# Optimization experiments

Hardware: AMD Instinct MI355X
Metric: run time of the kernel (lower is better)

Reference implementation:

```python
import jax, jax.numpy as jnp
import numpy as np

I, H, B, T, C = 256, 1024, 64, 256, 60


def setup_inputs() -> dict:
    key = jax.random.key(0)
    ks = jax.random.split(key, 7)
    s_ih = 1.0 / np.sqrt(H)
    return {
        "inputs": jax.random.normal(ks[0], (B, T, I), dtype=jnp.float32),
        "W_ih": jax.random.uniform(ks[1], (4 * H, I), jnp.float32, -s_ih, s_ih),
        "W_hh": jax.random.uniform(ks[2], (4 * H, H), jnp.float32, -s_ih, s_ih),
        "b_ih": jax.random.uniform(ks[3], (4 * H,), jnp.float32, -s_ih, s_ih),
        "b_hh": jax.random.uniform(ks[4], (4 * H,), jnp.float32, -s_ih, s_ih),
        "fc_w": jax.random.uniform(ks[5], (C, H), jnp.float32, -s_ih, s_ih),
        "fc_b": jax.random.uniform(ks[6], (C,), jnp.float32, -s_ih, s_ih),
    }


def reference(inputs, W_ih, W_hh, b_ih, b_hh, fc_w, fc_b):
    # Precompute input projections for all timesteps: [T, B, 4H]
    x_proj = jnp.einsum('bti,gi->tbg', inputs, W_ih) + b_ih + b_hh

    def step(carry, xg):
        h, c = carry
        gates = xg + h @ W_hh.T  # [B, 4H]
        i, f, g, o = jnp.split(gates, 4, axis=-1)  # PyTorch gate order i,f,g,o
        i = jax.nn.sigmoid(i)
        f = jax.nn.sigmoid(f)
        g = jnp.tanh(g)
        o = jax.nn.sigmoid(o)
        c_new = f * c + i * g
        h_new = o * jnp.tanh(c_new)
        return (h_new, c_new), None

    h0 = jnp.zeros((B, H), inputs.dtype)
    c0 = jnp.zeros((B, H), inputs.dtype)
    (h_last, _), _ = jax.lax.scan(step, (h0, c0), x_proj)

    logits = h_last @ fc_w.T + fc_b  # [B, C]
    return jax.nn.log_softmax(logits, axis=-1)
```

## Files before the change

### kernel.cpp

```cpp
#include <hip/hip_runtime.h>
#include <hip/hip_bf16.h>

typedef unsigned short u16;
typedef unsigned int u32;
typedef unsigned long long u64;
typedef __attribute__((ext_vector_type(8))) short short8;
typedef __attribute__((ext_vector_type(4))) float floatx4;

#define I_DIM 256
#define H_DIM 1024
#define B_DIM 64
#define T_DIM 256
#define C_DIM 60
#define NWG   128
#define UPW   8
#define BSTR  20
#define PACE  5

#define LDS_W_OFF    0
#define LDS_BIAS_OFF 81920
#define LDS_PACC_OFF 82048
#define LDS_FLAG_OFF 123008
#define LDS_TOTAL    123040

#define WS_XSWZ   0u
#define WS_HSWZ   8388608u
#define WS_HLAST  41943040u

#define LSBM 0x0001000100010001ull

__device__ __forceinline__ u16 f2bf(float f) {
    u32 u = __float_as_uint(f);
    u32 r = (u + 0x7fffu + ((u >> 16) & 1u)) >> 16;
    return (u16)r;
}
__device__ __forceinline__ float fsig(float x) { return 1.0f / (1.0f + __expf(-x)); }
__device__ __forceinline__ float ftanh(float x) { return 2.0f * fsig(2.0f * x) - 1.0f; }

union hfrag { short8 s; u64 q[2]; };

extern "C" __global__ void prep_x(const float* __restrict__ in, u16* __restrict__ xswz) {
    int o = blockIdx.x * 256 + threadIdx.x;
    int m = o & 15, q = (o >> 4) & 3, s = (o >> 6) & 7, mt = (o >> 9) & 3, t = o >> 11;
    int b = mt * 16 + m, k = s * 32 + q * 8;
    const float* src = in + ((size_t)(b * T_DIM + t)) * I_DIM + k;
    float4 v0 = *(const float4*)src;
    float4 v1 = *(const float4*)(src + 4);
    short8 val;
    val[0] = (short)f2bf(v0.x); val[1] = (short)f2bf(v0.y);
    val[2] = (short)f2bf(v0.z); val[3] = (short)f2bf(v0.w);
    val[4] = (short)f2bf(v1.x); val[5] = (short)f2bf(v1.y);
    val[6] = (short)f2bf(v1.z); val[7] = (short)f2bf(v1.w);
    *(short8*)(xswz + (size_t)o * 8) = val;
}

extern "C" __global__ void __launch_bounds__(512, 2) lstm_scan(
    const u16* __restrict__ xswz, u16* hswz,
    const float* __restrict__ Wih, const float* __restrict__ Whh,
    const float* __restrict__ bih, const float* __restrict__ bhh,
    float* hlast)
{
    extern __shared__ char lds[];
    u16*   Wlds = (u16*)(lds + LDS_W_OFF);
    float* bias = (float*)(lds + LDS_BIAS_OFF);
    float* pacc = (float*)(lds + LDS_PACC_OFF);
    int*   sbf  = (int*)(lds + LDS_FLAG_OFF);

    const int j    = blockIdx.x;
    const int tid  = threadIdx.x;
    const int lane = tid & 63;
    const int w    = tid >> 6;
    const int s    = w >> 1;
    const int ws   = w & 1;

    for (int i = 0; i < 10; ++i) {
        int wu = tid + i * 512;
        int nn = wu & 15, q = (wu >> 4) & 3, rest = wu >> 6;
        int sg = rest % 40, nt = rest / 40;
        int n = nt * 16 + nn;
        int g = n >> 3, uu = n & 7;
        int r = g * H_DIM + j * UPW + uu;
        int kb = sg * 32 + q * 8;
        const float* src = (kb < I_DIM) ? (Wih + (size_t)r * I_DIM + kb)
                                        : (Whh + (size_t)r * H_DIM + (kb - I_DIM));
        short8 val;
        #pragma unroll
        for (int e = 0; e < 8; ++e) val[e] = (short)f2bf(src[e]);
        *(short8*)(Wlds + (size_t)wu * 8) = val;
    }
    if (tid < 32) {
        int n = tid, g = n >> 3, uu = n & 7;
        int r = g * H_DIM + j * UPW + uu;
        bias[n] = bih[r] + bhh[r];
    }
    if (tid < 4) sbf[tid] = 0;
    __syncthreads();

    const int m16 = lane & 15, q4 = lane >> 4;
    const int sl    = ws * 64 + lane;
    const int pw_pm = sl >> 3;
    const int pw_uu = sl & 7;
    float creg = 0.0f;
    float* pacc_s = pacc + s * (2 * 64 * BSTR);
    int*   flag   = sbf + s;

    hfrag a[20];

    #pragma unroll
    for (int ss = 0; ss < 4; ++ss) {
        int sg = ws * 4 + ss;
        a[ss].s = *(const short8*)(xswz
            + (size_t)(((s * 8 + sg) * 4 + q4) * 16 + m16) * 8);
    }
    #pragma unroll
    for (int ss = 4; ss < 20; ++ss) {
        int sgh = ws * 16 + (ss - 4);
        a[ss].s = *(const short8*)(hswz
            + (size_t)(((s * 32 + sgh) * 4 + q4) * 16 + m16) * 8);
    }

    for (int t = 0; t < T_DIM; ++t) {
        const u16* hbase = hswz + (size_t)t * (B_DIM * H_DIM);
        u16*       hnext = hswz + (size_t)(t + 1) * (B_DIM * H_DIM);
        const u16* xnext = xswz + (size_t)(t + 1) * (B_DIM * I_DIM);
        const int  En    = (t % 13) + 1;
        const u64  Eq    = (u64)(En & 1) | ((u64)((En >> 1) & 1) << 16)
                         | ((u64)((En >> 2) & 1) << 32) | ((u64)((En >> 3) & 1) << 48);
        const int  Ep    = ((t + 1) % 13) + 1;

        floatx4 acc[2];
        acc[0] = (floatx4){0.f, 0.f, 0.f, 0.f};
        acc[1] = (floatx4){0.f, 0.f, 0.f, 0.f};
        #pragma unroll
        for (int ss = 0; ss < 4; ++ss) {
            int sg = ws * 4 + ss;
            #pragma unroll
            for (int nt = 0; nt < 2; ++nt) {
                short8 bv = *(const short8*)(Wlds
                    + (size_t)(((nt * 40 + sg) * 4 + q4) * 16 + m16) * 8);
                acc[nt] = __builtin_amdgcn_mfma_f32_16x16x32_bf16(
                    a[ss].s, bv, acc[nt], 0, 0, 0);
            }
        }

        if (t > 0) {
            u32 mk = 0;
            #pragma unroll
            for (int ss = 4; ss < 20; ++ss)
                if ((((a[ss].q[0] ^ Eq) | (a[ss].q[1] ^ Eq)) & LSBM) != 0)
                    mk |= 1u << ss;
            int rounds = 0;
            while (__any(mk != 0)) {
                ++rounds;
                #pragma unroll
                for (int ss = 4; ss < 20; ++ss)
                    if ((mk >> ss) & 1) {
                        int sgh = ws * 16 + (ss - 4);
                        const u64* pp = (const u64*)hbase
                            + (size_t)(((s * 32 + sgh) * 4 + q4) * 16 + m16) * 2;
                        a[ss].q[0] = __hip_atomic_load(pp,     __ATOMIC_RELAXED, __HIP_MEMORY_SCOPE_AGENT);
                        a[ss].q[1] = __hip_atomic_load(pp + 1, __ATOMIC_RELAXED, __HIP_MEMORY_SCOPE_AGENT);
                    }
                #pragma unroll
                for (int ss = 4; ss < 20; ++ss)
                    if (((mk >> ss) & 1) &&
                        ((((a[ss].q[0] ^ Eq) | (a[ss].q[1] ^ Eq)) & LSBM) == 0))
                        mk &= ~(1u << ss);
                if (__any(mk != 0)) {
                    if (rounds < 4) __builtin_amdgcn_s_sleep(4);
                    else            __builtin_amdgcn_s_sleep(16);
                }
            }
        }

        #pragma unroll
        for (int ss = 4; ss < 20; ++ss) {
            int sg = 8 + ws * 16 + (ss - 4);
            #pragma unroll
            for (int nt = 0; nt < 2; ++nt) {
                short8 bv = *(const short8*)(Wlds
                    + (size_t)(((nt * 40 + sg) * 4 + q4) * 16 + m16) * 8);
                acc[nt] = __builtin_amdgcn_mfma_f32_16x16x32_bf16(
                    a[ss].s, bv, acc[nt], 0, 0, 0);
            }
        }

        float* pc = pacc_s + (t & 1) * (64 * BSTR);
        #pragma unroll
        for (int nt = 0; nt < 2; ++nt)
            *(floatx4*)(pc + (ws * 32 + nt * 16 + m16) * BSTR + q4 * 4) = acc[nt];

        asm volatile("s_waitcnt lgkmcnt(0)" ::: "memory");
        if (lane == 0)
            __hip_atomic_fetch_add(flag, 1, __ATOMIC_RELAXED,
                                   __HIP_MEMORY_SCOPE_WORKGROUP);
        {
            const int tgt = 2 * (t + 1);
            while (__hip_atomic_load(flag, __ATOMIC_RELAXED,
                                     __HIP_MEMORY_SCOPE_WORKGROUP) < tgt)
                __builtin_amdgcn_s_sleep(1);
        }
        asm volatile("" ::: "memory");

        {
            float sv[4];
            #pragma unroll
            for (int g = 0; g < 4; ++g) {
                sv[g] = bias[g * 8 + pw_uu]
                      + pc[(g * 8 + pw_uu) * BSTR + pw_pm]
                      + pc[(32 + g * 8 + pw_uu) * BSTR + pw_pm];
            }
            float ig = fsig(sv[0]), fg = fsig(sv[1]), gg = ftanh(sv[2]), og = fsig(sv[3]);
            float c = fg * creg + ig * gg;
            creg = c;
            float h = og * ftanh(c);
            if (t == T_DIM - 1) {
                hlast[(size_t)(s * 16 + pw_pm) * H_DIM + j * UPW + pw_uu] = h;
            } else {
                u16 hb16 = (u16)((f2bf(h) & 0xFFFEu) | ((u32)(Ep >> (pw_uu & 3)) & 1u));
                u16* dst = hnext
                    + (size_t)((s * 32 + (j >> 2)) * 4 + (j & 3)) * 128 + sl;
                __hip_atomic_store(dst, hb16, __ATOMIC_RELAXED,
                                   __HIP_MEMORY_SCOPE_AGENT);
            }
        }
        asm volatile("" ::: "memory");

        if (t + 1 < T_DIM) {
            #pragma unroll
            for (int ss = 0; ss < 4; ++ss) {
                int sg = ws * 4 + ss;
                a[ss].s = *(const short8*)(xnext
                    + (size_t)(((s * 8 + sg) * 4 + q4) * 16 + m16) * 8);
            }
            for (int p = 0; p < PACE; ++p) __builtin_amdgcn_s_sleep(8);
            #pragma unroll
            for (int ss = 4; ss < 20; ++ss) {
                int sgh = ws * 16 + (ss - 4);
                a[ss].s = *(const short8*)(hnext
                    + (size_t)(((s * 32 + sgh) * 4 + q4) * 16 + m16) * 8);
            }
        }
    }
}

extern "C" __global__ void fc_logsoftmax(const float* __restrict__ hlast,
                                         const float* __restrict__ fcw,
                                         const float* __restrict__ fcb,
                                         float* __restrict__ out)
{
    int b = blockIdx.x, c = threadIdx.x;
    float acc = 0.0f;
    if (c < C_DIM) {
        const float* wr = fcw + (size_t)c * H_DIM;
        const float* hr = hlast + (size_t)b * H_DIM;
        for (int k = 0; k < H_DIM; k += 4) {
            float4 hv = *(const float4*)(hr + k);
            float4 wv = *(const float4*)(wr + k);
            acc += hv.x * wv.x + hv.y * wv.y + hv.z * wv.z + hv.w * wv.w;
        }
        acc += fcb[c];
    }
    float logit = (c < C_DIM) ? acc : -1e30f;
    float mx = logit;
    #pragma unroll
    for (int off = 32; off; off >>= 1) mx = fmaxf(mx, __shfl_xor(mx, off));
    float e = (c < C_DIM) ? expf(logit - mx) : 0.0f;
    float sum = e;
    #pragma unroll
    for (int off = 32; off; off >>= 1) sum += __shfl_xor(sum, off);
    if (c < C_DIM) out[b * C_DIM + c] = logit - mx - logf(sum);
}

extern "C" void kernel_launch(void* const* d_in, const int* in_sizes, int n_in,
                              void* d_out, int out_size, void* d_ws, size_t ws_size,
                              hipStream_t stream)
{
    const float* inputs = (const float*)d_in[0];
    const float* Wih    = (const float*)d_in[1];
    const float* Whh    = (const float*)d_in[2];
    const float* bih    = (const float*)d_in[3];
    const float* bhh    = (const float*)d_in[4];
    const float* fcw    = (const float*)d_in[5];
    const float* fcb    = (const float*)d_in[6];
    float* out = (float*)d_out;

    char* ws = (char*)d_ws;
    u16*   xswz  = (u16*)(ws + WS_XSWZ);
    u16*   hswz  = (u16*)(ws + WS_HSWZ);
    float* hlast = (float*)(ws + WS_HLAST);

    hipMemsetAsync(hswz, 0, B_DIM * H_DIM * sizeof(u16), stream);

    prep_x<<<2048, 256, 0, stream>>>(inputs, xswz);

    (void)hipFuncSetAttribute((const void*)lstm_scan,
                              hipFuncAttributeMaxDynamicSharedMemorySize, LDS_TOTAL);
    lstm_scan<<<NWG, 512, LDS_TOTAL, stream>>>(xswz, hswz, Wih, Whh, bih, bhh, hlast);
    fc_logsoftmax<<<B_DIM, 64, 0, stream>>>(hlast, fcw, fcb, out);
}
```

Before: 925.1 us.

## Split LSTM step K-reduction across four waves per batch slice

Doubles the workgroup to 1024 threads so each batch slice has four waves instead of two. The K dimension is split unevenly: wave 0 takes all input-projection slices plus two recurrent slices, and the other waves take ten recurrent slices each. This shortens the MFMA chain that waits on the freshly polled h. The double-buffered partial-sum LDS is replaced by a single buffer guarded by a second intra-slice barrier per step, which adds synchronization. Only half the lanes now do the pointwise update.

```diff
diff --git a/kernel.cpp b/kernel.cpp
--- a/kernel.cpp
+++ b/kernel.cpp
@@ -54,7 +54,7 @@
     *(short8*)(xswz + (size_t)o * 8) = val;
 }
 
-extern "C" __global__ void __launch_bounds__(512, 2) lstm_scan(
+extern "C" __global__ void __launch_bounds__(1024, 1) lstm_scan(
     const u16* __restrict__ xswz, u16* hswz,
     const float* __restrict__ Wih, const float* __restrict__ Whh,
     const float* __restrict__ bih, const float* __restrict__ bhh,
@@ -70,11 +70,11 @@
     const int tid  = threadIdx.x;
     const int lane = tid & 63;
     const int w    = tid >> 6;
-    const int s    = w >> 1;
-    const int ws   = w & 1;
-
-    for (int i = 0; i < 10; ++i) {
-        int wu = tid + i * 512;
+    const int s    = w >> 2;
+    const int ws   = w & 3;
+
+    for (int i = 0; i < 5; ++i) {
+        int wu = tid + i * 1024;
         int nn = wu & 15, q = (wu >> 4) & 3, rest = wu >> 6;
         int sg = rest % 40, nt = rest / 40;
         int n = nt * 16 + nn;
@@ -96,27 +96,23 @@
     if (tid < 4) sbf[tid] = 0;
     __syncthreads();
 
-    const int m16 = lane & 15, q4 = lane >> 4;
-    const int sl    = ws * 64 + lane;
-    const int pw_pm = sl >> 3;
-    const int pw_uu = sl & 7;
+    const int m16 = lane & 63 & 15, q4 = (lane & 63) >> 4;
+    const int item  = ws * 32 + (lane & 31);
+    const int pw_pm = item >> 3;
+    const int pw_uu = item & 7;
     float creg = 0.0f;
-    float* pacc_s = pacc + s * (2 * 64 * BSTR);
-    int*   flag   = sbf + s;
-
-    hfrag a[20];
+    float* pc   = pacc + s * (128 * BSTR);
+    int*   flag = sbf + s;
+
+    hfrag a[10];
 
     #pragma unroll
-    for (int ss = 0; ss < 4; ++ss) {
-        int sg = ws * 4 + ss;
-        a[ss].s = *(const short8*)(xswz
-            + (size_t)(((s * 8 + sg) * 4 + q4) * 16 + m16) * 8);
-    }
-    #pragma unroll
-    for (int ss = 4; ss < 20; ++ss) {
-        int sgh = ws * 16 + (ss - 4);
-        a[ss].s = *(const short8*)(hswz
-            + (size_t)(((s * 32 + sgh) * 4 + q4) * 16 + m16) * 8);
+    for (int ss = 0; ss < 10; ++ss) {
+        int sg = ws * 10 + ss;
+        const u16* src = (sg < 8)
+            ? xswz + (size_t)(((s * 8 + sg) * 4 + q4) * 16 + m16) * 8
+            : hswz + (size_t)(((s * 32 + (sg - 8)) * 4 + q4) * 16 + m16) * 8;
+        a[ss].s = *(const short8*)src;
     }
 
     for (int t = 0; t < T_DIM; ++t) {
@@ -131,38 +127,42 @@
         floatx4 acc[2];
         acc[0] = (floatx4){0.f, 0.f, 0.f, 0.f};
         acc[1] = (floatx4){0.f, 0.f, 0.f, 0.f};
-        #pragma unroll
-        for (int ss = 0; ss < 4; ++ss) {
-            int sg = ws * 4 + ss;
+
+        if (ws == 0) {
             #pragma unroll
-            for (int nt = 0; nt < 2; ++nt) {
-                short8 bv = *(const short8*)(Wlds
-                    + (size_t)(((nt * 40 + sg) * 4 + q4) * 16 + m16) * 8);
-                acc[nt] = __builtin_amdgcn_mfma_f32_16x16x32_bf16(
-                    a[ss].s, bv, acc[nt], 0, 0, 0);
+            for (int ss = 0; ss < 8; ++ss) {
+                #pragma unroll
+                for (int nt = 0; nt < 2; ++nt) {
+                    short8 bv = *(const short8*)(Wlds
+                        + (size_t)(((nt * 40 + ss) * 4 + q4) * 16 + m16) * 8);
+                    acc[nt] = __builtin_amdgcn_mfma_f32_16x16x32_bf16(
+                        a[ss].s, bv, acc[nt], 0, 0, 0);
+                }
             }
         }
 
         if (t > 0) {
             u32 mk = 0;
             #pragma unroll
-            for (int ss = 4; ss < 20; ++ss)
-                if ((((a[ss].q[0] ^ Eq) | (a[ss].q[1] ^ Eq)) & LSBM) != 0)
+            for (int ss = 0; ss < 10; ++ss)
+                if (ws * 10 + ss >= 8 &&
+                    ((((a[ss].q[0] ^ Eq) | (a[ss].q[1] ^ Eq)) & LSBM) != 0))
                     mk |= 1u << ss;
             int rounds = 0;
             while (__any(mk != 0)) {
                 ++rounds;
                 #pragma unroll
-                for (int ss = 4; ss < 20; ++ss)
-                    if ((mk >> ss) & 1) {
-                        int sgh = ws * 16 + (ss - 4);
+                for (int ss = 0; ss < 10; ++ss) {
+                    int sg = ws * 10 + ss;
+                    if (sg >= 8 && ((mk >> ss) & 1)) {
                         const u64* pp = (const u64*)hbase
-                            + (size_t)(((s * 32 + sgh) * 4 + q4) * 16 + m16) * 2;
+                            + (size_t)(((s * 32 + (sg - 8)) * 4 + q4) * 16 + m16) * 2;
                         a[ss].q[0] = __hip_atomic_load(pp,     __ATOMIC_RELAXED, __HIP_MEMORY_SCOPE_AGENT);
                         a[ss].q[1] = __hip_atomic_load(pp + 1, __ATOMIC_RELAXED, __HIP_MEMORY_SCOPE_AGENT);
                     }
-                #pragma unroll
-                for (int ss = 4; ss < 20; ++ss)
+                }
+                #pragma unroll
+                for (int ss = 0; ss < 10; ++ss)
                     if (((mk >> ss) & 1) &&
                         ((((a[ss].q[0] ^ Eq) | (a[ss].q[1] ^ Eq)) & LSBM) == 0))
                         mk &= ~(1u << ss);
@@ -174,18 +174,19 @@
         }
 
         #pragma unroll
-        for (int ss = 4; ss < 20; ++ss) {
-            int sg = 8 + ws * 16 + (ss - 4);
-            #pragma unroll
-            for (int nt = 0; nt < 2; ++nt) {
-                short8 bv = *(const short8*)(Wlds
-                    + (size_t)(((nt * 40 + sg) * 4 + q4) * 16 + m16) * 8);
-                acc[nt] = __builtin_amdgcn_mfma_f32_16x16x32_bf16(
-                    a[ss].s, bv, acc[nt], 0, 0, 0);
-            }
-        }
-
-        float* pc = pacc_s + (t & 1) * (64 * BSTR);
+        for (int ss = 0; ss < 10; ++ss) {
+            int sg = ws * 10 + ss;
+            if (sg >= 8) {
+                #pragma unroll
+                for (int nt = 0; nt < 2; ++nt) {
+                    short8 bv = *(const short8*)(Wlds
+                        + (size_t)(((nt * 40 + sg) * 4 + q4) * 16 + m16) * 8);
+                    acc[nt] = __builtin_amdgcn_mfma_f32_16x16x32_bf16(
+                        a[ss].s, bv, acc[nt], 0, 0, 0);
+                }
+            }
+        }
+
         #pragma unroll
         for (int nt = 0; nt < 2; ++nt)
             *(floatx4*)(pc + (ws * 32 + nt * 16 + m16) * BSTR + q4 * 4) = acc[nt];
@@ -195,20 +196,22 @@
             __hip_atomic_fetch_add(flag, 1, __ATOMIC_RELAXED,
                                    __HIP_MEMORY_SCOPE_WORKGROUP);
         {
-            const int tgt = 2 * (t + 1);
+            const int tgt = 8 * t + 4;
             while (__hip_atomic_load(flag, __ATOMIC_RELAXED,
                                      __HIP_MEMORY_SCOPE_WORKGROUP) < tgt)
                 __builtin_amdgcn_s_sleep(1);
         }
         asm volatile("" ::: "memory");
 
-        {
+        if ((lane & 63) < 32) {
             float sv[4];
             #pragma unroll
             for (int g = 0; g < 4; ++g) {
-                sv[g] = bias[g * 8 + pw_uu]
-                      + pc[(g * 8 + pw_uu) * BSTR + pw_pm]
-                      + pc[(32 + g * 8 + pw_uu) * BSTR + pw_pm];
+                float v = bias[g * 8 + pw_uu];
+                #pragma unroll
+                for (int ww = 0; ww < 4; ++ww)
+                    v += pc[(ww * 32 + g * 8 + pw_uu) * BSTR + pw_pm];
+                sv[g] = v;
             }
             float ig = fsig(sv[0]), fg = fsig(sv[1]), gg = ftanh(sv[2]), og = fsig(sv[3]);
             float c = fg * creg + ig * gg;
@@ -219,26 +222,38 @@
             } else {
                 u16 hb16 = (u16)((f2bf(h) & 0xFFFEu) | ((u32)(Ep >> (pw_uu & 3)) & 1u));
                 u16* dst = hnext
-                    + (size_t)((s * 32 + (j >> 2)) * 4 + (j & 3)) * 128 + sl;
+                    + (size_t)((s * 32 + (j >> 2)) * 4 + (j & 3)) * 128 + item;
                 __hip_atomic_store(dst, hb16, __ATOMIC_RELAXED,
                                    __HIP_MEMORY_SCOPE_AGENT);
             }
         }
+
         asm volatile("" ::: "memory");
+        if (lane == 0)
+            __hip_atomic_fetch_add(flag, 1, __ATOMIC_RELAXED,
+                                   __HIP_MEMORY_SCOPE_WORKGROUP);
+        {
+            const int tgt = 8 * t + 8;
+            while (__hip_atomic_load(flag, __ATOMIC_RELAXED,
+                                     __HIP_MEMORY_SCOPE_WORKGROUP) < tgt)
+                __builtin_amdgcn_s_sleep(1);
+        }
+        asm volatile("" ::: "memory");
 
         if (t + 1 < T_DIM) {
-            #pragma unroll
-            for (int ss = 0; ss < 4; ++ss) {
-                int sg = ws * 4 + ss;
-                a[ss].s = *(const short8*)(xnext
-                    + (size_t)(((s * 8 + sg) * 4 + q4) * 16 + m16) * 8);
+            if (ws == 0) {
+                #pragma unroll
+                for (int ss = 0; ss < 8; ++ss)
+                    a[ss].s = *(const short8*)(xnext
+                        + (size_t)(((s * 8 + ss) * 4 + q4) * 16 + m16) * 8);
             }
             for (int p = 0; p < PACE; ++p) __builtin_amdgcn_s_sleep(8);
             #pragma unroll
-            for (int ss = 4; ss < 20; ++ss) {
-                int sgh = ws * 16 + (ss - 4);
-                a[ss].s = *(const short8*)(hnext
-                    + (size_t)(((s * 32 + sgh) * 4 + q4) * 16 + m16) * 8);
+            for (int ss = 0; ss < 10; ++ss) {
+                int sg = ws * 10 + ss;
+                if (sg >= 8)
+                    a[ss].s = *(const short8*)(hnext
+                        + (size_t)(((s * 32 + (sg - 8)) * 4 + q4) * 16 + m16) * 8);
             }
         }
     }
@@ -296,6 +311,6 @@
 
     (void)hipFuncSetAttribute((const void*)lstm_scan,
                               hipFuncAttributeMaxDynamicSharedMemorySize, LDS_TOTAL);
-    lstm_scan<<<NWG, 512, LDS_TOTAL, stream>>>(xswz, hswz, Wih, Whh, bih, bhh, hlast);
+    lstm_scan<<<NWG, 1024, LDS_TOTAL, stream>>>(xswz, hswz, Wih, Whh, bih, bhh, hlast);
     fc_logsoftmax<<<B_DIM, 64, 0, stream>>>(hlast, fcw, fcb, out);
 }
```

Measured after the change: 1.424 ms. +53.9%, slower.

## Split each batch tile across two wave pairs with 1024-thread workgroups

Applied to the files above, without the earlier changes.

Doubles the workgroup to 1024 threads so each 16-row batch tile is handled by two wave groups, each owning 8 of the batch rows. Each group loads A fragments whose rows are remapped to its half. Every group still runs the full MFMA chain, but only the lanes whose output columns fall in its half write partial sums. Only 32 lanes per wave then run the gate math, which shortens the per-step serial critical path. The cost is redundant MFMA work, more LDS, one workgroup per CU instead of two, and more contention on the polled h buffer.

```diff
diff --git a/kernel.cpp b/kernel.cpp
--- a/kernel.cpp
+++ b/kernel.cpp
@@ -14,14 +14,14 @@
 #define C_DIM 60
 #define NWG   128
 #define UPW   8
-#define BSTR  20
+#define BSTR  12
 #define PACE  5
 
 #define LDS_W_OFF    0
 #define LDS_BIAS_OFF 81920
 #define LDS_PACC_OFF 82048
-#define LDS_FLAG_OFF 123008
-#define LDS_TOTAL    123040
+#define LDS_FLAG_OFF 131200
+#define LDS_TOTAL    131232
 
 #define WS_XSWZ   0u
 #define WS_HSWZ   8388608u
@@ -54,7 +54,7 @@
     *(short8*)(xswz + (size_t)o * 8) = val;
 }
 
-extern "C" __global__ void __launch_bounds__(512, 2) lstm_scan(
+extern "C" __global__ void __launch_bounds__(1024, 1) lstm_scan(
     const u16* __restrict__ xswz, u16* hswz,
     const float* __restrict__ Wih, const float* __restrict__ Whh,
     const float* __restrict__ bih, const float* __restrict__ bhh,
@@ -72,9 +72,11 @@
     const int w    = tid >> 6;
     const int s    = w >> 1;
     const int ws   = w & 1;
-
-    for (int i = 0; i < 10; ++i) {
-        int wu = tid + i * 512;
+    const int mt   = s >> 1;
+    const int half = s & 1;
+
+    for (int i = 0; i < 5; ++i) {
+        int wu = tid + i * 1024;
         int nn = wu & 15, q = (wu >> 4) & 3, rest = wu >> 6;
         int sg = rest % 40, nt = rest / 40;
         int n = nt * 16 + nn;
@@ -93,16 +95,19 @@
         int r = g * H_DIM + j * UPW + uu;
         bias[n] = bih[r] + bhh[r];
     }
-    if (tid < 4) sbf[tid] = 0;
+    if (tid < 8) sbf[tid] = 0;
     __syncthreads();
 
     const int m16 = lane & 15, q4 = lane >> 4;
-    const int sl    = ws * 64 + lane;
-    const int pw_pm = sl >> 3;
-    const int pw_uu = sl & 7;
+    const int em  = half * 8 + (m16 & 7);
+    const int cq  = q4 - 2 * half;
+    const int item  = ws * 32 + (lane & 31);
+    const int pw_pm = item >> 3;
+    const int pw_uu = item & 7;
+    const int pw_m  = half * 8 + pw_pm;
     float creg = 0.0f;
-    float* pacc_s = pacc + s * (2 * 64 * BSTR);
-    int*   flag   = sbf + s;
+    float* pc_s = pacc + s * (2 * 64 * BSTR);
+    int*   flag = sbf + s;
 
     hfrag a[20];
 
@@ -110,13 +115,13 @@
     for (int ss = 0; ss < 4; ++ss) {
         int sg = ws * 4 + ss;
         a[ss].s = *(const short8*)(xswz
-            + (size_t)(((s * 8 + sg) * 4 + q4) * 16 + m16) * 8);
+            + (size_t)(((mt * 8 + sg) * 4 + q4) * 16 + m16) * 8);
     }
     #pragma unroll
     for (int ss = 4; ss < 20; ++ss) {
         int sgh = ws * 16 + (ss - 4);
         a[ss].s = *(const short8*)(hswz
-            + (size_t)(((s * 32 + sgh) * 4 + q4) * 16 + m16) * 8);
+            + (size_t)(((mt * 32 + sgh) * 4 + q4) * 16 + em) * 8);
     }
 
     for (int t = 0; t < T_DIM; ++t) {
@@ -157,7 +162,7 @@
                     if ((mk >> ss) & 1) {
                         int sgh = ws * 16 + (ss - 4);
                         const u64* pp = (const u64*)hbase
-                            + (size_t)(((s * 32 + sgh) * 4 + q4) * 16 + m16) * 2;
+                            + (size_t)(((mt * 32 + sgh) * 4 + q4) * 16 + em) * 2;
                         a[ss].q[0] = __hip_atomic_load(pp,     __ATOMIC_RELAXED, __HIP_MEMORY_SCOPE_AGENT);
                         a[ss].q[1] = __hip_atomic_load(pp + 1, __ATOMIC_RELAXED, __HIP_MEMORY_SCOPE_AGENT);
                     }
@@ -185,10 +190,12 @@
             }
         }
 
-        float* pc = pacc_s + (t & 1) * (64 * BSTR);
-        #pragma unroll
-        for (int nt = 0; nt < 2; ++nt)
-            *(floatx4*)(pc + (ws * 32 + nt * 16 + m16) * BSTR + q4 * 4) = acc[nt];
+        float* pc = pc_s + (t & 1) * (64 * BSTR);
+        if (cq >= 0 && cq < 2) {
+            #pragma unroll
+            for (int nt = 0; nt < 2; ++nt)
+                *(floatx4*)(pc + (ws * 32 + nt * 16 + m16) * BSTR + cq * 4) = acc[nt];
+        }
 
         asm volatile("s_waitcnt lgkmcnt(0)" ::: "memory");
         if (lane == 0)
@@ -202,7 +209,7 @@
         }
         asm volatile("" ::: "memory");
 
-        {
+        if ((lane & 63) < 32) {
             float sv[4];
             #pragma unroll
             for (int g = 0; g < 4; ++g) {
@@ -215,11 +222,12 @@
             creg = c;
             float h = og * ftanh(c);
             if (t == T_DIM - 1) {
-                hlast[(size_t)(s * 16 + pw_pm) * H_DIM + j * UPW + pw_uu] = h;
+                hlast[(size_t)(mt * 16 + pw_m) * H_DIM + j * UPW + pw_uu] = h;
             } else {
                 u16 hb16 = (u16)((f2bf(h) & 0xFFFEu) | ((u32)(Ep >> (pw_uu & 3)) & 1u));
                 u16* dst = hnext
-                    + (size_t)((s * 32 + (j >> 2)) * 4 + (j & 3)) * 128 + sl;
+                    + (size_t)(((mt * 32 + (j >> 2)) * 4 + (j & 3)) * 16 + pw_m) * 8
+                    + pw_uu;
                 __hip_atomic_store(dst, hb16, __ATOMIC_RELAXED,
                                    __HIP_MEMORY_SCOPE_AGENT);
             }
@@ -231,14 +239,14 @@
             for (int ss = 0; ss < 4; ++ss) {
                 int sg = ws * 4 + ss;
                 a[ss].s = *(const short8*)(xnext
-                    + (size_t)(((s * 8 + sg) * 4 + q4) * 16 + m16) * 8);
+                    + (size_t)(((mt * 8 + sg) * 4 + q4) * 16 + m16) * 8);
             }
             for (int p = 0; p < PACE; ++p) __builtin_amdgcn_s_sleep(8);
             #pragma unroll
             for (int ss = 4; ss < 20; ++ss) {
                 int sgh = ws * 16 + (ss - 4);
                 a[ss].s = *(const short8*)(hnext
-                    + (size_t)(((s * 32 + sgh) * 4 + q4) * 16 + m16) * 8);
+                    + (size_t)(((mt * 32 + sgh) * 4 + q4) * 16 + em) * 8);
             }
         }
     }
@@ -296,6 +304,6 @@
 
     (void)hipFuncSetAttribute((const void*)lstm_scan,
                               hipFuncAttributeMaxDynamicSharedMemorySize, LDS_TOTAL);
-    lstm_scan<<<NWG, 512, LDS_TOTAL, stream>>>(xswz, hswz, Wih, Whh, bih, bhh, hlast);
+    lstm_scan<<<NWG, 1024, LDS_TOTAL, stream>>>(xswz, hswz, Wih, Whh, bih, bhh, hlast);
     fc_logsoftmax<<<B_DIM, 64, 0, stream>>>(hlast, fcw, fcb, out);
 }
```

Measured after the change: 2.615 ms. 183% more time.

## Split each timestep into two half-batch phases to pipeline hidden-state exchange

Applied to the files above, without the earlier changes.

Each workgroup's 16-row batch slice is processed as two 8-row halves per timestep. Each half does its own MFMA pass, LDS partial reduction, flag barrier and gate update, and the second half's operands are loaded while the first half's results are being published. The goal is to let the cross-workgroup hidden-state handoff for one half overlap with compute on the other. The fixed sleep pacing is removed and the LDS partial buffer shrinks. In exchange, each MFMA pass only uses 8 useful rows of a 16-row tile, so tensor-core work per timestep doubles, and there are twice as many barriers and spin-waits.

```diff
diff --git a/kernel.cpp b/kernel.cpp
--- a/kernel.cpp
+++ b/kernel.cpp
@@ -14,14 +14,13 @@
 #define C_DIM 60
 #define NWG   128
 #define UPW   8
-#define BSTR  20
-#define PACE  5
+#define BSTR  12
 
 #define LDS_W_OFF    0
 #define LDS_BIAS_OFF 81920
 #define LDS_PACC_OFF 82048
-#define LDS_FLAG_OFF 123008
-#define LDS_TOTAL    123040
+#define LDS_FLAG_OFF 106624
+#define LDS_TOTAL    106640
 
 #define WS_XSWZ   0u
 #define WS_HSWZ   8388608u
@@ -97,148 +96,164 @@
     __syncthreads();
 
     const int m16 = lane & 15, q4 = lane >> 4;
-    const int sl    = ws * 64 + lane;
-    const int pw_pm = sl >> 3;
-    const int pw_uu = sl & 7;
-    float creg = 0.0f;
-    float* pacc_s = pacc + s * (2 * 64 * BSTR);
-    int*   flag   = sbf + s;
-
-    hfrag a[20];
-
-    #pragma unroll
-    for (int ss = 0; ss < 4; ++ss) {
-        int sg = ws * 4 + ss;
-        a[ss].s = *(const short8*)(xswz
-            + (size_t)(((s * 8 + sg) * 4 + q4) * 16 + m16) * 8);
-    }
-    #pragma unroll
-    for (int ss = 4; ss < 20; ++ss) {
-        int sgh = ws * 16 + (ss - 4);
-        a[ss].s = *(const short8*)(hswz
-            + (size_t)(((s * 32 + sgh) * 4 + q4) * 16 + m16) * 8);
+    const int itm   = ws * 32 + (lane & 31);
+    const int ib    = itm >> 3;
+    const int uu    = itm & 7;
+    float creg[2] = {0.0f, 0.0f};
+    float* pc_s = pacc + s * (2 * 64 * BSTR);
+    int*   flag = sbf + s;
+
+    hfrag a[2][20];
+
+    {
+        const int em0 = (m16 & 7);
+        #pragma unroll
+        for (int ss = 0; ss < 4; ++ss)
+            a[0][ss].s = *(const short8*)(xswz
+                + (size_t)(((s * 8 + ws * 4 + ss) * 4 + q4) * 16 + em0) * 8);
+        #pragma unroll
+        for (int ss = 4; ss < 20; ++ss)
+            a[0][ss].s = *(const short8*)(hswz
+                + (size_t)(((s * 32 + ws * 16 + (ss - 4)) * 4 + q4) * 16 + em0) * 8);
     }
 
     for (int t = 0; t < T_DIM; ++t) {
-        const u16* hbase = hswz + (size_t)t * (B_DIM * H_DIM);
-        u16*       hnext = hswz + (size_t)(t + 1) * (B_DIM * H_DIM);
-        const u16* xnext = xswz + (size_t)(t + 1) * (B_DIM * I_DIM);
+        const u16* hb_t  = hswz + (size_t)t * (B_DIM * H_DIM);
+        u16*       hb_t1 = hswz + (size_t)(t + 1) * (B_DIM * H_DIM);
+        const u16* xb_t  = xswz + (size_t)t * (B_DIM * I_DIM);
+        const u16* xb_t1 = xswz + (size_t)(t + 1) * (B_DIM * I_DIM);
         const int  En    = (t % 13) + 1;
         const u64  Eq    = (u64)(En & 1) | ((u64)((En >> 1) & 1) << 16)
                          | ((u64)((En >> 2) & 1) << 32) | ((u64)((En >> 3) & 1) << 48);
         const int  Ep    = ((t + 1) % 13) + 1;
 
-        floatx4 acc[2];
-        acc[0] = (floatx4){0.f, 0.f, 0.f, 0.f};
-        acc[1] = (floatx4){0.f, 0.f, 0.f, 0.f};
         #pragma unroll
-        for (int ss = 0; ss < 4; ++ss) {
-            int sg = ws * 4 + ss;
-            #pragma unroll
-            for (int nt = 0; nt < 2; ++nt) {
-                short8 bv = *(const short8*)(Wlds
-                    + (size_t)(((nt * 40 + sg) * 4 + q4) * 16 + m16) * 8);
-                acc[nt] = __builtin_amdgcn_mfma_f32_16x16x32_bf16(
-                    a[ss].s, bv, acc[nt], 0, 0, 0);
-            }
-        }
-
-        if (t > 0) {
-            u32 mk = 0;
-            #pragma unroll
-            for (int ss = 4; ss < 20; ++ss)
-                if ((((a[ss].q[0] ^ Eq) | (a[ss].q[1] ^ Eq)) & LSBM) != 0)
-                    mk |= 1u << ss;
-            int rounds = 0;
-            while (__any(mk != 0)) {
-                ++rounds;
-                #pragma unroll
-                for (int ss = 4; ss < 20; ++ss)
-                    if ((mk >> ss) & 1) {
-                        int sgh = ws * 16 + (ss - 4);
-                        const u64* pp = (const u64*)hbase
-                            + (size_t)(((s * 32 + sgh) * 4 + q4) * 16 + m16) * 2;
-                        a[ss].q[0] = __hip_atomic_load(pp,     __ATOMIC_RELAXED, __HIP_MEMORY_SCOPE_AGENT);
-                        a[ss].q[1] = __hip_atomic_load(pp + 1, __ATOMIC_RELAXED, __HIP_MEMORY_SCOPE_AGENT);
-                    }
-                #pragma unroll
-                for (int ss = 4; ss < 20; ++ss)
-                    if (((mk >> ss) & 1) &&
-                        ((((a[ss].q[0] ^ Eq) | (a[ss].q[1] ^ Eq)) & LSBM) == 0))
-                        mk &= ~(1u << ss);
-                if (__any(mk != 0)) {
-                    if (rounds < 4) __builtin_amdgcn_s_sleep(4);
-                    else            __builtin_amdgcn_s_sleep(16);
-                }
-            }
-        }
-
-        #pragma unroll
-        for (int ss = 4; ss < 20; ++ss) {
-            int sg = 8 + ws * 16 + (ss - 4);
-            #pragma unroll
-            for (int nt = 0; nt < 2; ++nt) {
-                short8 bv = *(const short8*)(Wlds
-                    + (size_t)(((nt * 40 + sg) * 4 + q4) * 16 + m16) * 8);
-                acc[nt] = __builtin_amdgcn_mfma_f32_16x16x32_bf16(
-                    a[ss].s, bv, acc[nt], 0, 0, 0);
-            }
-        }
-
-        float* pc = pacc_s + (t & 1) * (64 * BSTR);
-        #pragma unroll
-        for (int nt = 0; nt < 2; ++nt)
-            *(floatx4*)(pc + (ws * 32 + nt * 16 + m16) * BSTR + q4 * 4) = acc[nt];
-
-        asm volatile("s_waitcnt lgkmcnt(0)" ::: "memory");
-        if (lane == 0)
-            __hip_atomic_fetch_add(flag, 1, __ATOMIC_RELAXED,
-                                   __HIP_MEMORY_SCOPE_WORKGROUP);
-        {
-            const int tgt = 2 * (t + 1);
-            while (__hip_atomic_load(flag, __ATOMIC_RELAXED,
-                                     __HIP_MEMORY_SCOPE_WORKGROUP) < tgt)
-                __builtin_amdgcn_s_sleep(1);
-        }
-        asm volatile("" ::: "memory");
-
-        {
-            float sv[4];
-            #pragma unroll
-            for (int g = 0; g < 4; ++g) {
-                sv[g] = bias[g * 8 + pw_uu]
-                      + pc[(g * 8 + pw_uu) * BSTR + pw_pm]
-                      + pc[(32 + g * 8 + pw_uu) * BSTR + pw_pm];
-            }
-            float ig = fsig(sv[0]), fg = fsig(sv[1]), gg = ftanh(sv[2]), og = fsig(sv[3]);
-            float c = fg * creg + ig * gg;
-            creg = c;
-            float h = og * ftanh(c);
-            if (t == T_DIM - 1) {
-                hlast[(size_t)(s * 16 + pw_pm) * H_DIM + j * UPW + pw_uu] = h;
-            } else {
-                u16 hb16 = (u16)((f2bf(h) & 0xFFFEu) | ((u32)(Ep >> (pw_uu & 3)) & 1u));
-                u16* dst = hnext
-                    + (size_t)((s * 32 + (j >> 2)) * 4 + (j & 3)) * 128 + sl;
-                __hip_atomic_store(dst, hb16, __ATOMIC_RELAXED,
-                                   __HIP_MEMORY_SCOPE_AGENT);
-            }
-        }
-        asm volatile("" ::: "memory");
-
-        if (t + 1 < T_DIM) {
+        for (int hh = 0; hh < 2; ++hh) {
+            const int em = hh * 8 + (m16 & 7);
+
+            floatx4 acc[2];
+            acc[0] = (floatx4){0.f, 0.f, 0.f, 0.f};
+            acc[1] = (floatx4){0.f, 0.f, 0.f, 0.f};
             #pragma unroll
             for (int ss = 0; ss < 4; ++ss) {
                 int sg = ws * 4 + ss;
-                a[ss].s = *(const short8*)(xnext
-                    + (size_t)(((s * 8 + sg) * 4 + q4) * 16 + m16) * 8);
-            }
-            for (int p = 0; p < PACE; ++p) __builtin_amdgcn_s_sleep(8);
+                #pragma unroll
+                for (int nt = 0; nt < 2; ++nt) {
+                    short8 bv = *(const short8*)(Wlds
+                        + (size_t)(((nt * 40 + sg) * 4 + q4) * 16 + m16) * 8);
+                    acc[nt] = __builtin_amdgcn_mfma_f32_16x16x32_bf16(
+                        a[hh][ss].s, bv, acc[nt], 0, 0, 0);
+                }
+            }
+
+            if (t > 0) {
+                u32 mk = 0;
+                #pragma unroll
+                for (int ss = 4; ss < 20; ++ss)
+                    if ((((a[hh][ss].q[0] ^ Eq) | (a[hh][ss].q[1] ^ Eq)) & LSBM) != 0)
+                        mk |= 1u << ss;
+                int rounds = 0;
+                while (__any(mk != 0)) {
+                    ++rounds;
+                    #pragma unroll
+                    for (int ss = 4; ss < 20; ++ss)
+                        if ((mk >> ss) & 1) {
+                            int sgh = ws * 16 + (ss - 4);
+                            const u64* pp = (const u64*)hb_t
+                                + (size_t)(((s * 32 + sgh) * 4 + q4) * 16 + em) * 2;
+                            a[hh][ss].q[0] = __hip_atomic_load(pp,     __ATOMIC_RELAXED, __HIP_MEMORY_SCOPE_AGENT);
+                            a[hh][ss].q[1] = __hip_atomic_load(pp + 1, __ATOMIC_RELAXED, __HIP_MEMORY_SCOPE_AGENT);
+                        }
+                    #pragma unroll
+                    for (int ss = 4; ss < 20; ++ss)
+                        if (((mk >> ss) & 1) &&
+                            ((((a[hh][ss].q[0] ^ Eq) | (a[hh][ss].q[1] ^ Eq)) & LSBM) == 0))
+                            mk &= ~(1u << ss);
+                    if (__any(mk != 0)) {
+                        if (rounds < 4) __builtin_amdgcn_s_sleep(4);
+                        else            __builtin_amdgcn_s_sleep(16);
+                    }
+                }
+            }
+
             #pragma unroll
             for (int ss = 4; ss < 20; ++ss) {
-                int sgh = ws * 16 + (ss - 4);
-                a[ss].s = *(const short8*)(hnext
-                    + (size_t)(((s * 32 + sgh) * 4 + q4) * 16 + m16) * 8);
+                int sg = 8 + ws * 16 + (ss - 4);
+                #pragma unroll
+                for (int nt = 0; nt < 2; ++nt) {
+                    short8 bv = *(const short8*)(Wlds
+                        + (size_t)(((nt * 40 + sg) * 4 + q4) * 16 + m16) * 8);
+                    acc[nt] = __builtin_amdgcn_mfma_f32_16x16x32_bf16(
+                        a[hh][ss].s, bv, acc[nt], 0, 0, 0);
+                }
+            }
+
+            float* pc = pc_s + hh * (64 * BSTR);
+            if (q4 < 2) {
+                #pragma unroll
+                for (int nt = 0; nt < 2; ++nt)
+                    *(floatx4*)(pc + (ws * 32 + nt * 16 + m16) * BSTR + q4 * 4) = acc[nt];
+            }
+
+            asm volatile("s_waitcnt lgkmcnt(0)" ::: "memory");
+            if (lane == 0)
+                __hip_atomic_fetch_add(flag, 1, __ATOMIC_RELAXED,
+                                       __HIP_MEMORY_SCOPE_WORKGROUP);
+            {
+                const int tgt = 2 * (2 * t + hh + 1);
+                while (__hip_atomic_load(flag, __ATOMIC_RELAXED,
+                                         __HIP_MEMORY_SCOPE_WORKGROUP) < tgt)
+                    __builtin_amdgcn_s_sleep(1);
+            }
+            asm volatile("" ::: "memory");
+
+            if (hh == 0) {
+                const int emo = 8 + (m16 & 7);
+                #pragma unroll
+                for (int ss = 0; ss < 4; ++ss)
+                    a[1][ss].s = *(const short8*)(xb_t
+                        + (size_t)(((s * 8 + ws * 4 + ss) * 4 + q4) * 16 + emo) * 8);
+                #pragma unroll
+                for (int ss = 4; ss < 20; ++ss)
+                    a[1][ss].s = *(const short8*)(hb_t
+                        + (size_t)(((s * 32 + ws * 16 + (ss - 4)) * 4 + q4) * 16 + emo) * 8);
+            }
+
+            if (lane < 32) {
+                float sv[4];
+                #pragma unroll
+                for (int g = 0; g < 4; ++g) {
+                    sv[g] = bias[g * 8 + uu]
+                          + pc[(g * 8 + uu) * BSTR + ib]
+                          + pc[(32 + g * 8 + uu) * BSTR + ib];
+                }
+                float ig = fsig(sv[0]), fg = fsig(sv[1]), gg = ftanh(sv[2]), og = fsig(sv[3]);
+                float c = fg * creg[hh] + ig * gg;
+                creg[hh] = c;
+                float h = og * ftanh(c);
+                if (t == T_DIM - 1) {
+                    hlast[(size_t)(s * 16 + hh * 8 + ib) * H_DIM + j * UPW + uu] = h;
+                } else {
+                    u16 hb16 = (u16)((f2bf(h) & 0xFFFEu) | ((u32)(Ep >> (uu & 3)) & 1u));
+                    u16* dst = hb_t1
+                        + (size_t)((s * 32 + (j >> 2)) * 4 + (j & 3)) * 128
+                        + hh * 64 + itm;
+                    __hip_atomic_store(dst, hb16, __ATOMIC_RELAXED,
+                                       __HIP_MEMORY_SCOPE_AGENT);
+                }
+            }
+            asm volatile("" ::: "memory");
+
+            if (hh == 1 && t + 1 < T_DIM) {
+                const int emo = (m16 & 7);
+                #pragma unroll
+                for (int ss = 0; ss < 4; ++ss)
+                    a[0][ss].s = *(const short8*)(xb_t1
+                        + (size_t)(((s * 8 + ws * 4 + ss) * 4 + q4) * 16 + emo) * 8);
+                #pragma unroll
+                for (int ss = 4; ss < 20; ++ss)
+                    a[0][ss].s = *(const short8*)(hb_t1
+                        + (size_t)(((s * 32 + ws * 16 + (ss - 4)) * 4 + q4) * 16 + emo) * 8);
             }
         }
     }
```

New measurement: 3.390 ms. 266% more time.
